# Kernel optimization log

Hardware: AMD Instinct MI355X
Metric: run time of the kernel (lower is better)

The kernel has to match this reference:

```python
import jax, jax.numpy as jnp
import numpy as np

NUM_HEADS = 16
D_ATT = 64


def setup_inputs() -> dict:
    key = jax.random.key(0)
    ks = jax.random.split(key, 7)
    b, n, hd = 4, 2048, NUM_HEADS * 64  # input last dim = num_heads * per-head embed_dim
    Q_vec = jax.random.normal(ks[0], (b, n, hd), dtype=jnp.float32)
    K_vec = jax.random.normal(ks[1], (b, n, hd), dtype=jnp.float32)
    V_vec = jax.random.normal(ks[2], (b, n, hd), dtype=jnp.float32)
    # torch Linear weights: [out_features, in_features] = [d_attention, per_head_dim]
    W_Q = jax.random.normal(ks[3], (D_ATT, 64), dtype=jnp.float32) * 0.02
    W_K = jax.random.normal(ks[4], (D_ATT, 64), dtype=jnp.float32) * 0.02
    W_V = jax.random.normal(ks[5], (D_ATT, 64), dtype=jnp.float32) * 0.02
    mask = jax.random.bernoulli(ks[6], p=0.9, shape=(b, n))  # bool [b, n]
    return {"Q_vec": Q_vec, "K_vec": K_vec, "V_vec": V_vec,
            "W_Q": W_Q, "W_K": W_K, "W_V": W_V, "mask": mask}


def reference(Q_vec, K_vec, V_vec, W_Q, W_K, W_V, mask):
    b, n, _ = Q_vec.shape
    h = NUM_HEADS
    scaling = 1.0 / np.sqrt(D_ATT).astype(np.float32)

    def split_heads(x):  # b n (h d) -> b h n d
        return x.reshape(b, n, h, -1).transpose(0, 2, 1, 3)

    # Linear applied per-head (weights are [out, in]; y = x @ W^T)
    q = split_heads(Q_vec) @ W_Q.T  # [b,h,n,D_ATT]
    k = split_heads(K_vec) @ W_K.T
    v = split_heads(V_vec) @ W_V.T

    dots = jnp.einsum('bhid,bhjd->bhij', q, k) * scaling  # [b,h,n,n]
    pair_mask = mask[:, None, :] & mask[:, :, None]       # [b,n,n]
    mask_value = -jnp.finfo(dots.dtype).max
    dots = jnp.where(pair_mask[:, None, :, :], dots, mask_value)
    attn = jax.nn.softmax(dots, axis=-1)
    out = jnp.einsum('bhij,bhjd->bhid', attn, v)          # [b,h,n,D_ATT]
    return out.transpose(0, 2, 1, 3).reshape(b, n, h * D_ATT)
```

## Files before the change

kernel.cpp:

```cpp
#include <hip/hip_runtime.h>

#define B_  4
#define N_  2048
#define H_  16
#define HD_ 1024

typedef short  bf16x8 __attribute__((ext_vector_type(8)));
typedef short  bf16x4 __attribute__((ext_vector_type(4)));
typedef float  f32x4  __attribute__((ext_vector_type(4)));

static __device__ __forceinline__ unsigned short f2bf(float f) {
    unsigned int u = __builtin_bit_cast(unsigned int, f);
    return (unsigned short)((u + 0x8000u) >> 16);
}
static __device__ __forceinline__ unsigned f2bf2pack(float lo, float hi) {
    unsigned a = __builtin_bit_cast(unsigned, lo) + 0x8000u;
    unsigned b = __builtin_bit_cast(unsigned, hi) + 0x8000u;
    return __builtin_amdgcn_perm(b, a, 0x07060302u);
}

__global__ __launch_bounds__(256) void proj_kernel(
    const float* __restrict__ Qv, const float* __restrict__ Kv,
    const float* __restrict__ Vv, const float* __restrict__ WQ,
    const float* __restrict__ WK, const float* __restrict__ WV,
    unsigned short* __restrict__ qs, unsigned short* __restrict__ ks,
    unsigned short* __restrict__ vt)
{
    __shared__ __align__(16) unsigned short xb[64][72];
    __shared__ __align__(16) unsigned short Wb[64][72];
    unsigned short (*sb)[72] = xb;

    const int tid  = threadIdx.x;
    const int wq   = tid >> 6;
    const int lane = tid & 63;
    const int l15  = lane & 15;
    const int quad = lane >> 4;

    const int i0 = blockIdx.x * 64;
    const int h  = blockIdx.y;
    const int bz = blockIdx.z;
    const int b  = bz / 3;
    const int p  = bz - b * 3;

    const size_t inbase = ((size_t)b * N_ + i0) * HD_ + h * 64;
    const size_t bh     = (size_t)b * H_ + h;

    const float* W   = (p == 0) ? WQ : (p == 1) ? WK : WV;
    const float* inp = ((p == 0) ? Qv : (p == 1) ? Kv : Vv) + inbase;

    for (int v = tid; v < 1024; v += 256) {
        int tok = v >> 4, c4 = (v & 15) * 4;
        float4 f = *reinterpret_cast<const float4*>(inp + (size_t)tok * HD_ + c4);
        uint2 u;
        u.x = f2bf2pack(f.x, f.y);
        u.y = f2bf2pack(f.z, f.w);
        *reinterpret_cast<uint2*>(&xb[tok][c4]) = u;
        float4 g = *reinterpret_cast<const float4*>(W + (size_t)v * 4);
        uint2 w2;
        w2.x = f2bf2pack(g.x, g.y);
        w2.y = f2bf2pack(g.z, g.w);
        *reinterpret_cast<uint2*>(&Wb[tok][c4]) = w2;
    }
    __syncthreads();

    bf16x8 ax[2];
    #pragma unroll
    for (int kh = 0; kh < 2; ++kh)
        ax[kh] = *reinterpret_cast<const bf16x8*>(&xb[wq * 16 + l15][kh * 32 + quad * 8]);

    f32x4 C[4];
    #pragma unroll
    for (int t = 0; t < 4; ++t) {
        C[t] = f32x4{0.f, 0.f, 0.f, 0.f};
        #pragma unroll
        for (int kh = 0; kh < 2; ++kh) {
            bf16x8 bw = *reinterpret_cast<const bf16x8*>(&Wb[t * 16 + l15][kh * 32 + quad * 8]);
            C[t] = __builtin_amdgcn_mfma_f32_16x16x32_bf16(ax[kh], bw, C[t], 0, 0, 0);
        }
    }

    __syncthreads();

    if (p < 2) {
        const float scl = (p == 0) ? 0.180336880f : 1.f;
        #pragma unroll
        for (int t = 0; t < 4; ++t)
            #pragma unroll
            for (int r = 0; r < 4; ++r)
                sb[wq * 16 + quad * 4 + r][t * 16 + l15] = f2bf(C[t][r] * scl);
        __syncthreads();
        unsigned short* dst = ((p == 0) ? qs : ks) + ((size_t)bh * N_ + i0) * 64;
        for (int v = tid; v < 512; v += 256) {
            int row = v >> 3, c0 = (v & 7) * 8;
            *reinterpret_cast<uint4*>(dst + (size_t)row * 64 + c0) =
                *reinterpret_cast<const uint4*>(&sb[row][c0]);
        }
    } else {
        #pragma unroll
        for (int t = 0; t < 4; ++t) {
            uint2 u;
            u.x = f2bf2pack(C[t][0], C[t][1]);
            u.y = f2bf2pack(C[t][2], C[t][3]);
            *reinterpret_cast<uint2*>(&sb[t * 16 + l15][wq * 16 + quad * 4]) = u;
        }
        __syncthreads();
        unsigned short* vdst = vt + (size_t)bh * 64 * N_ + i0;
        for (int v = tid; v < 512; v += 256) {
            int d = v >> 3, c0 = (v & 7) * 8;
            *reinterpret_cast<uint4*>(vdst + (size_t)d * N_ + c0) =
                *reinterpret_cast<const uint4*>(&sb[d][c0]);
        }
    }
}

__global__ __launch_bounds__(256) void attn_kernel(
    const unsigned short* __restrict__ qs, const unsigned short* __restrict__ ks,
    const unsigned short* __restrict__ vt, const int* __restrict__ maskp,
    float* __restrict__ out)
{
    __shared__ __align__(16) unsigned short Ks[64][72];
    __shared__ __align__(16) unsigned short Vt[64][68];
    __shared__ float kb[64];

    const int tid  = threadIdx.x;
    const int w    = tid >> 6;
    const int lane = tid & 63;
    const int l15  = lane & 15;
    const int quad = lane >> 4;

    const int lin  = blockIdx.y * gridDim.x + blockIdx.x;
    const int xcd  = lin & 7;
    const int idx  = lin >> 3;
    const int bh   = xcd * 8 + (idx >> 4);
    const int xblk = idx & 15;

    const int i0 = xblk * 128;
    const int b  = bh >> 4;
    const int h  = bh & 15;
    const int qrow0 = i0 + w * 32;

    bf16x8 aq[2][2];
    float  qm[2];
    #pragma unroll
    for (int rt = 0; rt < 2; ++rt) {
        const unsigned short* qrow = qs + ((size_t)bh * N_ + qrow0 + rt * 16 + l15) * 64;
        aq[rt][0] = *reinterpret_cast<const bf16x8*>(qrow + quad * 8);
        aq[rt][1] = *reinterpret_cast<const bf16x8*>(qrow + 32 + quad * 8);
        qm[rt] = maskp[b * N_ + qrow0 + rt * 16 + l15] ? 1.f : 0.f;
    }

    bf16x8 aones;
    #pragma unroll
    for (int j = 0; j < 8; ++j) aones[j] = (short)0x3F80;

    f32x4 O[2][4];
    f32x4 L[2];
    #pragma unroll
    for (int rt = 0; rt < 2; ++rt) {
        L[rt] = f32x4{0.f, 0.f, 0.f, 0.f};
        #pragma unroll
        for (int c = 0; c < 4; ++c) O[rt][c] = f32x4{0.f, 0.f, 0.f, 0.f};
    }

    const unsigned short* kbase = ks + (size_t)bh * N_ * 64;
    const unsigned short* vbase = vt + (size_t)bh * 64 * N_;

    for (int kv0 = 0; kv0 < N_; kv0 += 64) {
        __syncthreads();
        #pragma unroll
        for (int it = 0; it < 2; ++it) {
            int idx2 = tid + it * 256;
            int r = idx2 >> 3, g = idx2 & 7;
            *reinterpret_cast<uint4*>(&Ks[r][g * 8]) =
                *reinterpret_cast<const uint4*>(kbase + (size_t)(kv0 + r) * 64 + g * 8);
        }
        #pragma unroll
        for (int it = 0; it < 4; ++it) {
            int idx2 = tid + it * 256;
            int r = idx2 >> 4, g2 = idx2 & 15;
            *reinterpret_cast<uint2*>(&Vt[r][g2 * 4]) =
                *reinterpret_cast<const uint2*>(vbase + (size_t)r * N_ + kv0 + g2 * 4);
        }
        if (tid < 64) kb[tid] = maskp[b * N_ + kv0 + tid] ? 0.f : -1e30f;
        __syncthreads();

        bf16x8 ak[4][2];
        #pragma unroll
        for (int ct = 0; ct < 4; ++ct)
            #pragma unroll
            for (int kh = 0; kh < 2; ++kh)
                ak[ct][kh] = *reinterpret_cast<const bf16x8*>(&Ks[ct * 16 + l15][kh * 32 + quad * 8]);

        bf16x8 av[4][2];
        #pragma unroll
        for (int ct = 0; ct < 4; ++ct)
            #pragma unroll
            for (int kh = 0; kh < 2; ++kh) {
                bf16x4 lo = *reinterpret_cast<const bf16x4*>(&Vt[ct * 16 + l15][kh * 32 + quad * 4]);
                bf16x4 hi = *reinterpret_cast<const bf16x4*>(&Vt[ct * 16 + l15][kh * 32 + 16 + quad * 4]);
                av[ct][kh] = bf16x8{lo[0], lo[1], lo[2], lo[3], hi[0], hi[1], hi[2], hi[3]};
            }

        f32x4 kbv[4];
        #pragma unroll
        for (int ct = 0; ct < 4; ++ct)
            kbv[ct] = *reinterpret_cast<const f32x4*>(&kb[ct * 16 + quad * 4]);

        #pragma unroll
        for (int rt = 0; rt < 2; ++rt) {
            f32x4 S[4];
            #pragma unroll
            for (int ct = 0; ct < 4; ++ct) {
                S[ct] = kbv[ct];
                #pragma unroll
                for (int kh = 0; kh < 2; ++kh)
                    S[ct] = __builtin_amdgcn_mfma_f32_16x16x32_bf16(ak[ct][kh], aq[rt][kh], S[ct], 0, 0, 0);
            }
            unsigned pk[4][2];
            #pragma unroll
            for (int ct = 0; ct < 4; ++ct) {
                float e0 = __builtin_amdgcn_exp2f(S[ct][0] * qm[rt]);
                float e1 = __builtin_amdgcn_exp2f(S[ct][1] * qm[rt]);
                float e2 = __builtin_amdgcn_exp2f(S[ct][2] * qm[rt]);
                float e3 = __builtin_amdgcn_exp2f(S[ct][3] * qm[rt]);
                pk[ct][0] = f2bf2pack(e0, e1);
                pk[ct][1] = f2bf2pack(e2, e3);
            }
            bf16x8 ap[2];
            #pragma unroll
            for (int kh = 0; kh < 2; ++kh) {
                uint4 u = uint4{pk[2 * kh][0], pk[2 * kh][1], pk[2 * kh + 1][0], pk[2 * kh + 1][1]};
                ap[kh] = __builtin_bit_cast(bf16x8, u);
            }
            #pragma unroll
            for (int kh = 0; kh < 2; ++kh)
                L[rt] = __builtin_amdgcn_mfma_f32_16x16x32_bf16(aones, ap[kh], L[rt], 0, 0, 0);
            #pragma unroll
            for (int ct = 0; ct < 4; ++ct)
                #pragma unroll
                for (int kh = 0; kh < 2; ++kh)
                    O[rt][ct] = __builtin_amdgcn_mfma_f32_16x16x32_bf16(av[ct][kh], ap[kh], O[rt][ct], 0, 0, 0);
        }
    }

    #pragma unroll
    for (int rt = 0; rt < 2; ++rt) {
        float inv = 1.f / L[rt][0];
        float* orow = out + ((size_t)b * N_ + qrow0 + rt * 16 + l15) * HD_ + h * 64 + quad * 4;
        #pragma unroll
        for (int ct = 0; ct < 4; ++ct)
            #pragma unroll
            for (int r = 0; r < 4; ++r)
                orow[ct * 16 + r] = O[rt][ct][r] * inv;
    }
}

extern "C" void kernel_launch(void* const* d_in, const int* in_sizes, int n_in,
                              void* d_out, int out_size, void* d_ws, size_t ws_size,
                              hipStream_t stream)
{
    const float* Qv  = (const float*)d_in[0];
    const float* Kv  = (const float*)d_in[1];
    const float* Vv  = (const float*)d_in[2];
    const float* WQ  = (const float*)d_in[3];
    const float* WK  = (const float*)d_in[4];
    const float* WV  = (const float*)d_in[5];
    const int*   msk = (const int*)d_in[6];
    float* out = (float*)d_out;

    const size_t per = (size_t)B_ * H_ * N_ * 64;
    unsigned short* qsb = (unsigned short*)d_ws;
    unsigned short* ksb = qsb + per;
    unsigned short* vtb = ksb + per;

    proj_kernel<<<dim3(N_ / 64, H_, B_ * 3), 256, 0, stream>>>(Qv, Kv, Vv, WQ, WK, WV, qsb, ksb, vtb);
    attn_kernel<<<dim3(N_ / 128, B_ * H_), 256, 0, stream>>>(qsb, ksb, vtb, msk, out);
}
```

Baseline: 238.7 us.

## Double-buffer K/V tiles with register prefetch in attention kernel

Adds a second LDS buffer for the K, V and mask-bias tiles. The next tile is loaded from global memory into registers before the current tile's MFMA work and written to the other buffer afterwards, so each step needs one barrier instead of two. This is meant to hide global-load latency behind the compute. It costs roughly double the shared memory plus extra registers per thread, which may lower occupancy. The final step also fetches a redundant wrapped-around tile.

Result: slower. 251.2 us (+5.2%).

```diff
diff --git a/kernel.cpp b/kernel.cpp
--- a/kernel.cpp
+++ b/kernel.cpp
@@ -118,9 +118,9 @@
     const unsigned short* __restrict__ vt, const int* __restrict__ maskp,
     float* __restrict__ out)
 {
-    __shared__ __align__(16) unsigned short Ks[64][72];
-    __shared__ __align__(16) unsigned short Vt[64][68];
-    __shared__ float kb[64];
+    __shared__ __align__(16) unsigned short Ks[2][64][72];
+    __shared__ __align__(16) unsigned short Vt[2][64][68];
+    __shared__ __align__(16) float kb[2][64];
 
     const int tid  = threadIdx.x;
     const int w    = tid >> 6;
@@ -165,46 +165,59 @@
     const unsigned short* kbase = ks + (size_t)bh * N_ * 64;
     const unsigned short* vbase = vt + (size_t)bh * 64 * N_;
 
-    for (int kv0 = 0; kv0 < N_; kv0 += 64) {
-        __syncthreads();
+    #pragma unroll
+    for (int it = 0; it < 2; ++it) {
+        int idx2 = tid + it * 256, r = idx2 >> 3, g = idx2 & 7;
+        *reinterpret_cast<uint4*>(&Ks[0][r][g * 8]) =
+            *reinterpret_cast<const uint4*>(kbase + (size_t)r * 64 + g * 8);
+    }
+    #pragma unroll
+    for (int it = 0; it < 4; ++it) {
+        int idx2 = tid + it * 256, r = idx2 >> 4, g2 = idx2 & 15;
+        *reinterpret_cast<uint2*>(&Vt[0][r][g2 * 4]) =
+            *reinterpret_cast<const uint2*>(vbase + (size_t)r * N_ + g2 * 4);
+    }
+    if (tid < 64) kb[0][tid] = maskp[b * N_ + tid] ? 0.f : -1e30f;
+    __syncthreads();
+
+    auto tile_step = [&](int kv0, int cur, int nb) __attribute__((always_inline)) {
+        const int kvn = (kv0 + 64) & (N_ - 1);
+        uint4 kreg[2];
         #pragma unroll
         for (int it = 0; it < 2; ++it) {
-            int idx2 = tid + it * 256;
-            int r = idx2 >> 3, g = idx2 & 7;
-            *reinterpret_cast<uint4*>(&Ks[r][g * 8]) =
-                *reinterpret_cast<const uint4*>(kbase + (size_t)(kv0 + r) * 64 + g * 8);
-        }
+            int idx2 = tid + it * 256, r = idx2 >> 3, g = idx2 & 7;
+            kreg[it] = *reinterpret_cast<const uint4*>(kbase + (size_t)(kvn + r) * 64 + g * 8);
+        }
+        uint2 vreg[4];
         #pragma unroll
         for (int it = 0; it < 4; ++it) {
-            int idx2 = tid + it * 256;
-            int r = idx2 >> 4, g2 = idx2 & 15;
-            *reinterpret_cast<uint2*>(&Vt[r][g2 * 4]) =
-                *reinterpret_cast<const uint2*>(vbase + (size_t)r * N_ + kv0 + g2 * 4);
-        }
-        if (tid < 64) kb[tid] = maskp[b * N_ + kv0 + tid] ? 0.f : -1e30f;
-        __syncthreads();
+            int idx2 = tid + it * 256, r = idx2 >> 4, g2 = idx2 & 15;
+            vreg[it] = *reinterpret_cast<const uint2*>(vbase + (size_t)r * N_ + kvn + g2 * 4);
+        }
+        float kmr = 0.f;
+        if (tid < 64) kmr = maskp[b * N_ + kvn + tid] ? 0.f : -1e30f;
 
         bf16x8 ak[4][2];
         #pragma unroll
         for (int ct = 0; ct < 4; ++ct)
             #pragma unroll
             for (int kh = 0; kh < 2; ++kh)
-                ak[ct][kh] = *reinterpret_cast<const bf16x8*>(&Ks[ct * 16 + l15][kh * 32 + quad * 8]);
+                ak[ct][kh] = *reinterpret_cast<const bf16x8*>(&Ks[cur][ct * 16 + l15][kh * 32 + quad * 8]);
 
         bf16x8 av[4][2];
         #pragma unroll
         for (int ct = 0; ct < 4; ++ct)
             #pragma unroll
             for (int kh = 0; kh < 2; ++kh) {
-                bf16x4 lo = *reinterpret_cast<const bf16x4*>(&Vt[ct * 16 + l15][kh * 32 + quad * 4]);
-                bf16x4 hi = *reinterpret_cast<const bf16x4*>(&Vt[ct * 16 + l15][kh * 32 + 16 + quad * 4]);
+                bf16x4 lo = *reinterpret_cast<const bf16x4*>(&Vt[cur][ct * 16 + l15][kh * 32 + quad * 4]);
+                bf16x4 hi = *reinterpret_cast<const bf16x4*>(&Vt[cur][ct * 16 + l15][kh * 32 + 16 + quad * 4]);
                 av[ct][kh] = bf16x8{lo[0], lo[1], lo[2], lo[3], hi[0], hi[1], hi[2], hi[3]};
             }
 
         f32x4 kbv[4];
         #pragma unroll
         for (int ct = 0; ct < 4; ++ct)
-            kbv[ct] = *reinterpret_cast<const f32x4*>(&kb[ct * 16 + quad * 4]);
+            kbv[ct] = *reinterpret_cast<const f32x4*>(&kb[cur][ct * 16 + quad * 4]);
 
         #pragma unroll
         for (int rt = 0; rt < 2; ++rt) {
@@ -241,6 +254,24 @@
                 for (int kh = 0; kh < 2; ++kh)
                     O[rt][ct] = __builtin_amdgcn_mfma_f32_16x16x32_bf16(av[ct][kh], ap[kh], O[rt][ct], 0, 0, 0);
         }
+
+        #pragma unroll
+        for (int it = 0; it < 2; ++it) {
+            int idx2 = tid + it * 256, r = idx2 >> 3, g = idx2 & 7;
+            *reinterpret_cast<uint4*>(&Ks[nb][r][g * 8]) = kreg[it];
+        }
+        #pragma unroll
+        for (int it = 0; it < 4; ++it) {
+            int idx2 = tid + it * 256, r = idx2 >> 4, g2 = idx2 & 15;
+            *reinterpret_cast<uint2*>(&Vt[nb][r][g2 * 4]) = vreg[it];
+        }
+        if (tid < 64) kb[nb][tid] = kmr;
+        __syncthreads();
+    };
+
+    for (int kv0 = 0; kv0 < N_; kv0 += 128) {
+        tile_step(kv0, 0, 1);
+        tile_step(kv0 + 64, 1, 0);
     }
 
     #pragma unroll
```
